# Optimization experiments

Measured on AMD Instinct MI355X. Metric: run time of the kernel, lower is better.

## Reference

```python
import jax, jax.numpy as jnp
import numpy as np

W_PRIOR_STD = 1.0          # w_prior_stddev
OBS_STD = 1.0              # observational_noise_stddev
EPS = 1e-7                 # keras backend.epsilon()
B, E, K, C = 64, 32, 128, 512


def setup_inputs() -> dict:
    key = jax.random.key(0)
    k1, k2, k3, k4 = jax.random.split(key, 4)
    x = jax.random.normal(k1, (B, E, C), jnp.float32)
    prior_memory_mean = jax.random.normal(k2, (K, C), jnp.float32)  # truncated_normal(0,1) init
    prior_log_variance_scale = jax.random.uniform(k3, (), jnp.float32)  # scalar weight (init zeros; nonzero for testing)
    log_w_stddev = jnp.float32(0.3)  # constant(initial_w_stddev) init
    z_noise = jax.random.normal(k4, (E, B, C), jnp.float32)  # reparam noise for z_distribution.sample()
    return {"x": x, "prior_memory_mean": prior_memory_mean,
            "prior_log_variance_scale": prior_log_variance_scale,
            "log_w_stddev": log_w_stddev, "z_noise": z_noise}


def _kl_w(w, sw, k):
    # KL( N(w, sw^2 I_k) || N(0, w_prior^2 I_k) ), w_prior = 1
    return 0.5 * (k * sw * sw + jnp.sum(w * w, axis=-1) - k - 2.0 * k * jnp.log(sw))


def reference(x, prior_memory_mean, prior_log_variance_scale, log_w_stddev, z_noise):
    b, e, c = x.shape
    k = prior_memory_mean.shape[0]
    dt = x.dtype
    sw = jnp.exp(log_w_stddev)                      # w_stddev
    lam = (OBS_STD ** 2) / (W_PRIOR_STD ** 2)       # l2 regularizer in w-solve
    I_k = jnp.eye(k, dtype=dt)

    # prior state (tiled over batch)
    M0 = jnp.broadcast_to(prior_memory_mean[None], (b, k, c)) + jnp.zeros((b, k, c), dt)
    var = prior_log_variance_scale + EPS
    U0 = jnp.broadcast_to(var * I_k, (b, k, k)) + jnp.zeros((b, k, k), dt)

    z = jnp.transpose(x, (1, 0, 2))  # [E,B,C]

    def solve_w(M, z_t):
        # least squares: w = (M M^T + lam I)^{-1} M z  -> [B,K]
        A = jnp.einsum('bkc,blc->bkl', M, M) + lam * I_k
        rhs = jnp.einsum('bkc,bc->bk', M, z_t)
        return jnp.linalg.solve(A, rhs[..., None])[..., 0]

    def step(carry, z_t):
        M, U = carry                                    # [B,K,C], [B,K,K]
        w = solve_w(M, z_t)                             # memory sample == mean; iteration_count == 1
        delta = z_t - jnp.einsum('bk,bkc->bc', w, M)    # prediction delta [B,C]
        wU = jnp.einsum('bk,bkl->bl', w, U)             # cross variance [B,K]
        sigma = jnp.sum(wU * w, axis=-1) + OBS_STD ** 2 # z episode covariance [B]
        gain = wU / sigma[:, None]                      # [B,K]
        M_new = M + gain[..., None] * delta[:, None, :] # rank-1 Kalman update
        U_new = U - jnp.einsum('bk,bl->bkl', gain, wU)
        return (M_new, U_new), _kl_w(w, sw, k)          # per-step w divergence [B]

    (M_post, U_post), kl_episode = jax.lax.scan(step, (M0, U0), z)  # kl_episode [E,B]

    # read memory: batched solve with shared Gram matrix over episode
    A = jnp.einsum('bkc,blc->bkl', M_post, M_post) + lam * I_k
    rhs = jnp.einsum('bkc,ebc->bke', M_post, z)
    w_read = jnp.transpose(jnp.linalg.solve(A, rhs), (2, 0, 1))     # [E,B,K]
    z_mean = jnp.einsum('ebk,bkc->ebc', w_read, M_post)
    kl_read = _kl_w(w_read, sw, k)                                  # [E,B]

    total_divergence = jnp.mean(kl_episode + kl_read)               # add_loss value
    z_sample = z_mean + OBS_STD * z_noise                           # reparameterized sample
    return jnp.transpose(z_sample, (1, 0, 2)), total_divergence
```

## Files before the change

kernel.cpp:

```cpp
#include <hip/hip_runtime.h>

#define BB 64
#define EE 32
#define KK 128
#define CC 512
#define V0EPS 1e-7f

#define LTR 132
#define PTS 132
#define LKM 36
#define L36 36
#define LWT 176
#define SEG(i) ((((i) >> 4) * 20) + ((i) & 15))

#define SC_S2  0
#define SC_SIG 1
#define SC_KL  2
#define SC_B1  3
#define SC_B2  4
#define SC_R11 5
#define SC_R12 6
#define SC_R22 7

__device__ __forceinline__ float wsum64(float v) {
#pragma unroll
  for (int m = 32; m >= 1; m >>= 1) v += __shfl_xor(v, m, 64);
  return v;
}

__device__ __forceinline__ float wsum32(float v) {
#pragma unroll
  for (int m = 16; m >= 1; m >>= 1) v += __shfl_xor(v, m, 64);
  return v;
// ... 203 lines not shown
          if (q == (j2 >> 4)) sFb[dn][i][r] = wv_;
          if (r == j2) {
#pragma unroll
            for (int c = 0; c < 16; c++) {
              sPv[dn][i][16 * q + c] = wreg[c];
              sPv[dn][i][128 + 16 * q + c] = vreg[c];
            }
          }
        }
      }
      __syncthreads();
    }
    {
      float dval = 0.0f;
#pragma unroll
      for (int c = 0; c < 16; c++) if (c == (r & 15)) dval = wreg[c];
      if (q == (r >> 4)) sFb[0][0][r] = dval;
    }
    __syncthreads();
    {
      const float sc = 1.0f / sFb[0][0][r];
      float4* o4 = (float4*)(Ainv0 + r * KK + 16 * q);
#pragma unroll
      for (int u = 0; u < 4; u++) {
        float4 o;
        o.x = vreg[4 * u] * sc; o.y = vreg[4 * u + 1] * sc;
        o.z = vreg[4 * u + 2] * sc; o.w = vreg[4 * u + 3] * sc;
        o4[u] = o;
      }
    }
  }
}

__global__ __launch_bounds__(512) void scan_kernel(
    const float* __restrict__ Pg, const float* __restrict__ Sg,
    const float* __restrict__ scaleP, const float* __restrict__ Ainv0,
    float* __restrict__ wsKL, float* __restrict__ wsKLr, float* __restrict__ wsWt) {
  __shared__ __align__(16) float sPT[EE * PTS];
  __shared__ __align__(16) float sGT[EE * LTR];
  __shared__ __align__(16) float sEggT[EE * LTR];
  __shared__ __align__(16) float uni2[EE * LTR];
  __shared__ __align__(16) float uni3[KK * LKM];
  __shared__ __align__(16) float uni1[KK * LKM];
  __shared__ __align__(16) float sEk[KK * LKM];
  __shared__ __align__(16) float sS[EE * L36];
  __shared__ __align__(16) float sD[EE * L36];
  __shared__ __align__(16) float sW[160];
  __shared__ __align__(16) float sWU[160];
  __shared__ __align__(16) float sPu[160];
  __shared__ __align__(16) float sPm[160];
  __shared__ __align__(16) float sQ[160];
  __shared__ __align__(16) float sDz[EE];
  __shared__ __align__(16) float sDgw[EE];
  __shared__ __align__(16) float sQt[EE];
  __shared__ __align__(16) float sScal[16];

  float* sYT = uni2;
  float* sGk = uni3;
  float* sYk = uni1;

  const int tid = threadIdx.x, wv = tid >> 6, ln = tid & 63;
  const int mr = tid >> 2, mq = tid & 3;
  const int b = blockIdx.x;

  float areg[32];
  {
    const float4* a4 = (const float4*)(Ainv0 + mr * KK + 32 * mq);
#pragma unroll
    for (int u = 0; u < 8; u++) {
      const float4 t4 = a4[u];
      areg[4 * u] = t4.x; areg[4 * u + 1] = t4.y; areg[4 * u + 2] = t4.z; areg[4 * u + 3] = t4.w;
    }
  }
  {
    const float* Pb = Pg + (size_t)b * KK * EE;
#pragma unroll
    for (int i = 0; i < 8; i++) {
      const int idx = tid + 512 * i;
      sPT[(idx & 31) * PTS + (idx >> 5)] = Pb[idx];
    }
    const float* Sb = Sg + (size_t)b * 4096;
#pragma unroll
    for (int i = 0; i < 2; i++) {
      const int idx = tid + 512 * i;
      sS[(idx >> 5) * L36 + (idx & 31)] =
          Sb[idx] + Sb[idx + 1024] + Sb[idx + 2048] + Sb[idx + 3072];
    }
  }
  if (tid < 16) sScal[tid] = 0.0f;
  const float v0 = scaleP[0] + V0EPS;
  __syncthreads();
  {
    const float* xb = sPT + 32 * mq;
    float s = 0;
#pragma unroll
    for (int c = 0; c < 32; c++) s += areg[c] * xb[c];
    s += __shfl_xor(s, 1, 64); s += __shfl_xor(s, 2, 64);
    if (mq == 0) sW[SEG(mr)] = s;
  }
  __syncthreads();

#pragma unroll 1
  for (int t = 0; t < EE; ++t) {
    const bool hn = (t + 1 < EE);
    {
      const float* xb = sW + 40 * mq;
      float s = 0;
#pragma unroll
      for (int c = 0; c < 16; c++) s += areg[c] * xb[c];
#pragma unroll
      for (int c = 0; c < 16; c++) s += areg[16 + c] * xb[20 + c];
      s += __shfl_xor(s, 1, 64); s += __shfl_xor(s, 2, 64);
      if (mq == 0) sPm[SEG(mr)] = s;
    }
    if (tid < 256) {
      const int s8 = tid >> 3, p3 = tid & 7;
      if (s8 < t) {
        const float* gr = sGT + s8 * LTR + 16 * p3;
        const float* wr_ = sW + 20 * p3;
        float s = 0;
#pragma unroll
        for (int kk = 0; kk < 16; kk++) s += gr[kk] * wr_[kk];
        s += __shfl_xor(s, 1, 64); s += __shfl_xor(s, 2, 64); s += __shfl_xor(s, 4, 64);
        if (p3 == 0) sDgw[s8] = s;
      } else if (s8 == 31) {
        const float* wp = sW + 20 * p3;
        float s = 0;
#pragma unroll
        for (int kk = 0; kk < 16; kk++) s += wp[kk] * wp[kk];
        s += __shfl_xor(s, 1, 64); s += __shfl_xor(s, 2, 64); s += __shfl_xor(s, 4, 64);
        if (p3 == 0) sScal[SC_S2] = s;
      }
    } else {
      const int j = (tid - 256) >> 3, p3 = tid & 7;
      if (j < t) {
        const float* yr = sYT + j * LTR + 16 * p3;
        const float* wr_ = sW + 20 * p3;
        float s = 0;
#pragma unroll
        for (int kk = 0; kk < 16; kk++) s += yr[kk] * wr_[kk];
        s += __shfl_xor(s, 1, 64); s += __shfl_xor(s, 2, 64); s += __shfl_xor(s, 4, 64);
        if (p3 == 0) sQt[j] = s;
      }
    }
    __syncthreads();
    if (tid < 256) {
      const int k = tid >> 1, h = tid & 1;
      const float* yk = sYk + k * LKM + 16 * h;
      const float* qb = sQt + 16 * h;
      float a = 0;
#pragma unroll
      for (int u = 0; u < 16; u++) {
        const int j = 16 * h + u;
        a += (j < t) ? yk[u] * qb[u] : 0.0f;
      }
      a += __shfl_xor(a, 1, 64);
      if (h == 0) sWU[SEG(k)] = v0 * sW[SEG(k)] - a;
    } else if (tid < 384) {
      const int k = tid - 256;
      float a = sW[SEG(k)];
      const float* ek = sEk + k * LKM;
      const int nc = (t + 3) >> 2;
#pragma unroll 1
      for (int c4 = 0; c4 < nc; ++c4) {
        const float4 ev = *(const float4*)(ek + 4 * c4);
        const float4 dv = *(const float4*)(sDgw + 4 * c4);
        const int u0 = 4 * c4;
        a -= ((u0 + 0 < t) ? ev.x * dv.x : 0.0f) + ((u0 + 1 < t) ? ev.y * dv.y : 0.0f) +
             ((u0 + 2 < t) ? ev.z * dv.z : 0.0f) + ((u0 + 3 < t) ? ev.w * dv.w : 0.0f);
      }
      sEk[k * LKM + t] = a;
      sEggT[t * LTR + k] = a;
    } else if (tid < 448) {
      if (ln < 32) {
        const int r2 = ln;
        float a = (r2 == t) ? 1.0f : 0.0f;
        for (int s2 = 0; s2 < t; ++s2) a -= sDgw[s2] * sD[s2 * L36 + r2];
        sD[t * L36 + r2] = a;
      } else {
        const int k0 = (ln - 32) * 4;
        const float4 wv4 = *(const float4*)(sW + SEG(k0));
        const float4 pm4 = *(const float4*)(sPm + SEG(k0));
        float a = dot4(wv4, pm4);
        a = wsum32(a);
        if (ln == 32) sScal[SC_R22] = a;
      }
    } else {
      const float s2v = sScal[SC_S2];
      float a = (ln < t) ? sQt[ln] * sQt[ln] : 0.0f;
      a = wsum64(a);
      if (ln == 0) {
        sScal[SC_SIG] = v0 * s2v - a + 1.0f;
        sScal[SC_KL] += s2v;
      }
    }
    __syncthreads();
    {
      const float* xb = sWU + 40 * mq;
      float s = 0;
#pragma unroll
      for (int c = 0; c < 16; c++) s += areg[c] * xb[c];
#pragma unroll
      for (int c = 0; c < 16; c++) s += areg[16 + c] * xb[20 + c];
      s += __shfl_xor(s, 1, 64); s += __shfl_xor(s, 2, 64);
      if (mq == 0) sPu[SEG(mr)] = s;
    }
    if (tid < 256) {
      const int s4 = tid >> 3, p3 = tid & 7;
      if (hn && s4 <= t) {
        const float* er = sEggT + s4 * LTR + 16 * p3;
        const float* pr = sPT + (t + 1) * PTS + 16 * p3;
        float a = 0;
#pragma unroll
        for (int kk = 0; kk < 16; kk++) a -= er[kk] * pr[kk];
        const float4 dv = *(const float4*)(sD + s4 * L36 + 4 * p3);
        const float4 sv = *(const float4*)(sS + (t + 1) * L36 + 4 * p3);
        a += dot4(dv, sv);
        a += __shfl_xor(a, 1, 64); a += __shfl_xor(a, 2, 64); a += __shfl_xor(a, 4, 64);
        if (p3 == 0) sDz[s4] = a;
      }
    } else if (tid < 320) {
      float a = sEggT[t * LTR + ln] * sPT[t * PTS + ln] +
                sEggT[t * LTR + ln + 64] * sPT[t * PTS + ln + 64];
      a = wsum64(a);
      if (ln == 0) sScal[SC_B2] = a;
    } else if (tid < 384) {
      if (ln < 32) {
        float a = sD[t * L36 + ln] * sS[t * L36 + ln];
        a = wsum32(a);
        if (ln == 0) sScal[SC_B1] = a;
      } else {
        const int k0 = (ln - 32) * 4;
        const float4 wu4 = *(const float4*)(sWU + SEG(k0));
        const float4 pm4 = *(const float4*)(sPm + SEG(k0));
        float a = dot4(wu4, pm4);
        a = wsum32(a);
        if (ln == 32) sScal[SC_R12] = a;
      }
    } else if (tid < 448) {
      const float sig = sScal[SC_SIG];
      const float rsq = rsqrtf(sig);
#pragma unroll
      for (int u = 0; u < 2; u++) {
        const int k = ln + 64 * u;
        const float wu = sWU[SEG(k)];
        const float gv = wu / sig;
        const float yv = wu * rsq;
        sGT[t * LTR + k] = gv;
        sGk[k * LKM + t] = gv;
        sYT[t * LTR + k] = yv;
        sYk[k * LKM + t] = yv;
      }
    }
    __syncthreads();
    if (hn) {
      const float* gk = sGk + mr * LKM + 8 * mq;
      const float* dzb = sDz + 8 * mq;
      float a = 0;
#pragma unroll
      for (int u = 0; u < 8; u++) {
        const int s2 = 8 * mq + u;
        a += (s2 < t) ? gk[u] * dzb[u] : 0.0f;
      }
      a += __shfl_xor(a, 1, 64); a += __shfl_xor(a, 2, 64);
      if (mq == 0)
        sQ[SEG(mr)] = sPT[(t + 1) * PTS + mr] + a + (sWU[SEG(mr)] / sScal[SC_SIG]) * sDz[t];
    }
    if (wv == 0) {
      float a = sWU[SEG(ln)] * sPu[SEG(ln)] + sWU[SEG(ln + 64)] * sPu[SEG(ln + 64)];
      a = wsum64(a);
      if (ln == 0) sScal[SC_R11] = a;
    }
    __syncthreads();
    {
      const float4 sc0 = *(const float4*)(sScal);
      const float4 sc1 = *(const float4*)(sScal + 4);
      const float rs = 1.0f / sc0.y;
      const float beta = sc0.w - sc1.x - sc0.x;
      const float e11 = sc1.y * rs * rs;
      const float e12 = sc1.z * rs + 1.0f;
      const float e22 = sc1.w - beta;
      const float rd = 1.0f / (e11 * e22 - e12 * e12);
      const float t11 = e22 * rd, t12 = -e12 * rd, t22 = e11 * rd;
      const float u1r = sPu[SEG(mr)] * rs, u2r = sPm[SEG(mr)];
      const float* pub = sPu + 40 * mq;
      const float* pmb = sPm + 40 * mq;
#pragma unroll
      for (int c = 0; c < 16; c++) {
        const float u1c = pub[c] * rs;
        const float u2c = pmb[c];
        areg[c] -= u1r * (t11 * u1c + t12 * u2c) + u2r * (t12 * u1c + t22 * u2c);
      }
#pragma unroll
      for (int c = 0; c < 16; c++) {
        const float u1c = pub[20 + c] * rs;
        const float u2c = pmb[20 + c];
        areg[16 + c] -= u1r * (t11 * u1c + t12 * u2c) + u2r * (t12 * u1c + t22 * u2c);
      }
    }
    if (hn) {
      const float* xb = sQ + 40 * mq;
      float s = 0;
#pragma unroll
      for (int c = 0; c < 16; c++) s += areg[c] * xb[c];
#pragma unroll
      for (int c = 0; c < 16; c++) s += areg[16 + c] * xb[20 + c];
      s += __shfl_xor(s, 1, 64); s += __shfl_xor(s, 2, 64);
      if (mq == 0) sW[SEG(mr)] = s;
    }
    __syncthreads();
  }

  float* sR1T  = uni2;
  float* sGamT = uni2 + 1152;
  float* sRhsT = uni1;
  float* sWrT  = uni3;
  if (tid == 0) wsKL[b] = sScal[SC_KL];

#pragma unroll
  for (int h = 0; h < 2; ++h) {
    const int lin = tid + 512 * h, s = lin >> 5, e = lin & 31;
    const float4* er = (const float4*)(sEggT + s * LTR);
    const float4* pr = (const float4*)(sPT + e * PTS);
    float a = 0;
#pragma unroll 8
    for (int u = 0; u < 32; ++u) a -= dot4(er[u], pr[u]);
    const float4* dr = (const float4*)(sD + s * L36);
    const float4* sr = (const float4*)(sS + e * L36);
#pragma unroll
    for (int u = 0; u < 8; ++u) a += dot4(dr[u], sr[u]);
    sR1T[e * 36 + s] = a;
  }
  __syncthreads();
  {
    const int k = tid & 127, e4 = tid >> 7;
    float4 g0, g1, g2, g3, g4, g5, g6, g7;
    {
      const float4* gk = (const float4*)(sGk + k * LKM);
      g0 = gk[0]; g1 = gk[1]; g2 = gk[2]; g3 = gk[3];
      g4 = gk[4]; g5 = gk[5]; g6 = gk[6]; g7 = gk[7];
    }
#pragma unroll
    for (int u = 0; u < 8; ++u) {
      const int e = e4 * 8 + u;
      const float4* r1 = (const float4*)(sR1T + e * 36);
      float a = sPT[e * PTS + k];
      a += dot4(g0, r1[0]) + dot4(g1, r1[1]) + dot4(g2, r1[2]) + dot4(g3, r1[3]);
      a += dot4(g4, r1[4]) + dot4(g5, r1[5]) + dot4(g6, r1[6]) + dot4(g7, r1[7]);
      sRhsT[e * PTS + k] = a;
    }
  }
  __syncthreads();
#pragma unroll 2
  for (int e = 0; e < EE; ++e) {
    const float* xb = sRhsT + e * PTS + 32 * mq;
    float s = 0;
#pragma unroll
    for (int c = 0; c < 32; c++) s += areg[c] * xb[c];
    s += __shfl_xor(s, 1, 64); s += __shfl_xor(s, 2, 64);
    if (mq == 0) sWrT[e * PTS + mr] = s;
  }
  __syncthreads();
#pragma unroll
  for (int h = 0; h < 2; ++h) {
    const int lin = tid + 512 * h, s = lin >> 5, e = lin & 31;
    const float4* gr = (const float4*)(sGT + s * LTR);
    const float4* wr = (const float4*)(sWrT + e * PTS);
    float a = 0;
#pragma unroll 8
    for (int u = 0; u < 32; ++u) a += dot4(gr[u], wr[u]);
    sGamT[e * 36 + s] = a;
  }
  __syncthreads();
  {
    const int k = tid & 127, e4 = tid >> 7;
    float4 E0, E1, E2, E3, E4, E5, E6, E7;
    {
      const float4* ek = (const float4*)(sEk + k * LKM);
      E0 = ek[0]; E1 = ek[1]; E2 = ek[2]; E3 = ek[3];
      E4 = ek[4]; E5 = ek[5]; E6 = ek[6]; E7 = ek[7];
    }
#pragma unroll
    for (int u = 0; u < 8; ++u) {
      const int e = e4 * 8 + u;
      const float4* gm = (const float4*)(sGamT + e * 36);
      float a = sWrT[e * PTS + k];
      a -= dot4(E0, gm[0]) + dot4(E1, gm[1]) + dot4(E2, gm[2]) + dot4(E3, gm[3]);
      a -= dot4(E4, gm[4]) + dot4(E5, gm[5]) + dot4(E6, gm[6]) + dot4(E7, gm[7]);
      wsWt[(size_t)b * 5120 + e * 160 + k] = a;
    }
  }
  {
    const int e = tid & 31, sp = tid >> 5;
    float4 gm[8];
    {
      const float4* g4 = (const float4*)(sGamT + e * 36);
#pragma unroll
      for (int u = 0; u < 8; ++u) gm[u] = g4[u];
    }
#pragma unroll
    for (int h = 0; h < 2; ++h) {
      const int sp2 = sp + 16 * h;
      float a = 0;
#pragma unroll
      for (int u = 0; u < 8; ++u) {
        const float4 g = gm[u];
        a += sD[(4 * u + 0) * L36 + sp2] * g.x + sD[(4 * u + 1) * L36 + sp2] * g.y +
             sD[(4 * u + 2) * L36 + sp2] * g.z + sD[(4 * u + 3) * L36 + sp2] * g.w;
      }
      wsWt[(size_t)b * 5120 + e * 160 + 128 + sp2] = a;
    }
  }
  {
    const int e = tid >> 4, p = tid & 15;
    const float4* wr = (const float4*)(sWrT + e * PTS + 8 * p);
    const float4 w0 = wr[0], w1 = wr[1];
    float a = dot4(w0, w0) + dot4(w1, w1);
    a += __shfl_xor(a, 1, 64); a += __shfl_xor(a, 2, 64);
    a += __shfl_xor(a, 4, 64); a += __shfl_xor(a, 8, 64);
    if (p == 0) wsKLr[b * EE + e] = a;
  }
}

__global__ __launch_bounds__(512) void postBF_kernel(
    const float* __restrict__ wsWt, const float* __restrict__ x,
    const float* __restrict__ M0, const float* __restrict__ znoise,
    const float* __restrict__ wsKL, const float* __restrict__ wsKLr,
    const float* __restrict__ lwsP, float* __restrict__ out) {
  __shared__ __align__(16) float sWtT[32 * LWT];
  __shared__ __align__(16) float Mch[2 * 16 * 132];
  const int tid = threadIdx.x;

  if (blockIdx.x == 256) {
    float* sPp = sWtT;
    float s = 0.0f;
    if (tid < 64) s += wsKL[tid];
    for (int i = tid; i < 2048; i += 512) s += wsKLr[i];
    sPp[tid] = s;
    __syncthreads();
    for (int off = 256; off > 0; off >>= 1) {
      if (tid < off) sPp[tid] += sPp[tid + off];
      __syncthreads();
    }
    if (tid == 0) {
      const float lws = lwsP[0];
      const float sw2 = expf(2.0f * lws);
      out[(size_t)BB * EE * CC] =
          0.5f * sPp[0] / (float)(EE * BB) + (float)KK * (sw2 - 1.0f - 2.0f * lws);
    }
    return;
  }

  const int b = blockIdx.x >> 2, cq = blockIdx.x & 3;
  {
    const int e = tid >> 4, j = tid & 15;
    const float* Wg = wsWt + (size_t)b * 5120 + e * 160;
#pragma unroll
    for (int u = 0; u < 10; ++u) sWtT[e * LWT + j + 16 * u] = Wg[j + 16 * u];
  }
  const int srow = tid >> 5, sc4 = tid & 31;
  const int e = tid & 31, cs = tid >> 5;
  const float* xb = x + (size_t)b * EE * CC;
  const int cbase = cq * 128;
  float4 st = *(const float4*)(M0 + srow * CC + cbase + 4 * sc4);
  float acc[8];
#pragma unroll
  for (int u = 0; u < 8; u++) acc[u] = 0.0f;
  int buf = 0;
#pragma unroll 1
  for (int ch2 = 0; ch2 < 10; ++ch2) {
    *(float4*)(Mch + buf * 2112 + srow * 132 + 4 * sc4) = st;
    __syncthreads();
    if (ch2 + 1 < 10) {
      const int row = (ch2 + 1) * 16 + srow;
      st = (row < 128) ? *(const float4*)(M0 + row * CC + cbase + 4 * sc4)
                       : *(const float4*)(xb + (row - 128) * CC + cbase + 4 * sc4);
    }
    const float4* wt4 = (const float4*)(sWtT + e * LWT + ch2 * 16);
    const float4 wa = wt4[0], wb = wt4[1], wc = wt4[2], wd = wt4[3];
    const float wv16[16] = {wa.x, wa.y, wa.z, wa.w, wb.x, wb.y, wb.z, wb.w,
                            wc.x, wc.y, wc.z, wc.w, wd.x, wd.y, wd.z, wd.w};
#pragma unroll
    for (int kk = 0; kk < 16; ++kk) {
      const float* mrp = Mch + buf * 2112 + kk * 132 + cs * 8;
      const float4 m0 = *(const float4*)(mrp);
      const float4 m1 = *(const float4*)(mrp + 4);
      const float wk = wv16[kk];
      acc[0] += wk * m0.x; acc[1] += wk * m0.y; acc[2] += wk * m0.z; acc[3] += wk * m0.w;
      acc[4] += wk * m1.x; acc[5] += wk * m1.y; acc[6] += wk * m1.z; acc[7] += wk * m1.w;
    }
    buf ^= 1;
  }
  {
    const size_t ob = ((size_t)b * EE + e) * CC + cbase + cs * 8;
    const size_t nb = ((size_t)e * BB + b) * CC + cbase + cs * 8;
#pragma unroll
    for (int u = 0; u < 2; u++) {
      const float4 nz = *(const float4*)(znoise + nb + 4 * u);
      float4 o;
      o.x = acc[4 * u] + nz.x;     o.y = acc[4 * u + 1] + nz.y;
      o.z = acc[4 * u + 2] + nz.z; o.w = acc[4 * u + 3] + nz.w;
      *(float4*)(out + ob + 4 * u) = o;
    }
  }
}

extern "C" void kernel_launch(void* const* d_in, const int* in_sizes, int n_in,
                              void* d_out, int out_size, void* d_ws, size_t ws_size,
                              hipStream_t stream) {
  (void)in_sizes; (void)n_in; (void)out_size; (void)ws_size;
  const float* x = (const float*)d_in[0];
  const float* M0 = (const float*)d_in[1];
  const float* scaleP = (const float*)d_in[2];
  const float* lwsP = (const float*)d_in[3];
  const float* znoise = (const float*)d_in[4];
  float* out = (float*)d_out;

  float* ws = (float*)d_ws;
  float* wsP = ws;
  float* wsSp = wsP + 262144;
  float* wsA0 = wsSp + 262144;
  float* wsAinv0 = wsA0 + 16384;
  float* wsKL = wsAinv0 + 16384;
  float* wsKLr = wsKL + 64;
  float* wsWt = wsKLr + 2048;

  a0_kernel<<<512, 256, 0, stream>>>(M0, wsA0);
  psinv_kernel<<<257, 1024, 0, stream>>>(x, M0, wsP, wsSp, wsA0, wsAinv0);
  scan_kernel<<<BB, 512, 0, stream>>>(wsP, wsSp, scaleP, wsAinv0,
                                      wsKL, wsKLr, wsWt);
  postBF_kernel<<<257, 512, 0, stream>>>(wsWt, x, M0, znoise, wsKL, wsKLr, lwsP, out);
}
```

Measured before the change: 261.6 us.

## Fuse scan and post kernels into one cooperative launch with grid sync

Merges the per-batch scan kernel and the post-processing read/output kernel into a single cooperative kernel of 256 blocks, with the first 64 blocks running the scan and all blocks doing the output GEMM after a grid-wide barrier. Shared memory is carved from a single unified array so both phases can reuse it. The aim is to remove one kernel launch and its inter-kernel gap. In exchange it adds grid-sync overhead and requires all 256 blocks to be co-resident, and the post blocks now carry the scan kernel's large shared memory footprint.

```diff
diff --git a/kernel.cpp b/kernel.cpp
--- a/kernel.cpp
+++ b/kernel.cpp
@@ -1,4 +1,7 @@
 #include <hip/hip_runtime.h>
+#include <hip/hip_cooperative_groups.h>
+
+namespace cg = cooperative_groups;
 
 #define BB 64
 #define EE 32
@@ -268,407 +271,465 @@
   }
 }
 
-__global__ __launch_bounds__(512) void scan_kernel(
+__global__ __launch_bounds__(512) void scanpost_kernel(
     const float* __restrict__ Pg, const float* __restrict__ Sg,
     const float* __restrict__ scaleP, const float* __restrict__ Ainv0,
-    float* __restrict__ wsKL, float* __restrict__ wsKLr, float* __restrict__ wsWt) {
-  __shared__ __align__(16) float sPT[EE * PTS];
-  __shared__ __align__(16) float sGT[EE * LTR];
-  __shared__ __align__(16) float sEggT[EE * LTR];
-  __shared__ __align__(16) float uni2[EE * LTR];
-  __shared__ __align__(16) float uni3[KK * LKM];
-  __shared__ __align__(16) float uni1[KK * LKM];
-  __shared__ __align__(16) float sEk[KK * LKM];
-  __shared__ __align__(16) float sS[EE * L36];
-  __shared__ __align__(16) float sD[EE * L36];
-  __shared__ __align__(16) float sW[160];
-  __shared__ __align__(16) float sWU[160];
-  __shared__ __align__(16) float sPu[160];
-  __shared__ __align__(16) float sPm[160];
-  __shared__ __align__(16) float sQ[160];
-  __shared__ __align__(16) float sDz[EE];
-  __shared__ __align__(16) float sDgw[EE];
-  __shared__ __align__(16) float sQt[EE];
-  __shared__ __align__(16) float sScal[16];
-
-  float* sYT = uni2;
-  float* sGk = uni3;
-  float* sYk = uni1;
-
-  const int tid = threadIdx.x, wv = tid >> 6, ln = tid & 63;
-  const int mr = tid >> 2, mq = tid & 3;
-  const int b = blockIdx.x;
-
-  float areg[32];
-  {
-    const float4* a4 = (const float4*)(Ainv0 + mr * KK + 32 * mq);
-#pragma unroll
-    for (int u = 0; u < 8; u++) {
-      const float4 t4 = a4[u];
-      areg[4 * u] = t4.x; areg[4 * u + 1] = t4.y; areg[4 * u + 2] = t4.z; areg[4 * u + 3] = t4.w;
-    }
-  }
-  {
-    const float* Pb = Pg + (size_t)b * KK * EE;
-#pragma unroll
-    for (int i = 0; i < 8; i++) {
-      const int idx = tid + 512 * i;
-      sPT[(idx & 31) * PTS + (idx >> 5)] = Pb[idx];
-    }
-    const float* Sb = Sg + (size_t)b * 4096;
-#pragma unroll
-    for (int i = 0; i < 2; i++) {
-      const int idx = tid + 512 * i;
-      sS[(idx >> 5) * L36 + (idx & 31)] =
-          Sb[idx] + Sb[idx + 1024] + Sb[idx + 2048] + Sb[idx + 3072];
-    }
-  }
-  if (tid < 16) sScal[tid] = 0.0f;
-  const float v0 = scaleP[0] + V0EPS;
-  __syncthreads();
-  {
-    const float* xb = sPT + 32 * mq;
-    float s = 0;
-#pragma unroll
-    for (int c = 0; c < 32; c++) s += areg[c] * xb[c];
-    s += __shfl_xor(s, 1, 64); s += __shfl_xor(s, 2, 64);
-    if (mq == 0) sW[SEG(mr)] = s;
-  }
-  __syncthreads();
-
-#pragma unroll 1
-  for (int t = 0; t < EE; ++t) {
-    const bool hn = (t + 1 < EE);
-    {
-      const float* xb = sW + 40 * mq;
+    float* __restrict__ wsKL, float* __restrict__ wsKLr, float* __restrict__ wsWt,
+    const float* __restrict__ x, const float* __restrict__ M0,
+    const float* __restrict__ znoise, const float* __restrict__ lwsP,
+    float* __restrict__ out) {
+  __shared__ __align__(16) float SM[33936];
+  const int tid = threadIdx.x;
+
+  if (blockIdx.x < 64) {
+    float* sPT   = SM;
+    float* sGT   = SM + 4224;
+    float* sEggT = SM + 8448;
+    float* uni2  = SM + 12672;
+    float* uni3  = SM + 16896;
+    float* uni1  = SM + 21504;
+    float* sEk   = SM + 26112;
+    float* sS    = SM + 30720;
+    float* sD    = SM + 31872;
+    float* sW    = SM + 33024;
+    float* sWU   = SM + 33184;
+    float* sPu   = SM + 33344;
+    float* sPm   = SM + 33504;
+    float* sQ    = SM + 33664;
+    float* sDz   = SM + 33824;
+    float* sDgw  = SM + 33856;
+    float* sQt   = SM + 33888;
+    float* sScal = SM + 33920;
+    float* sYT = uni2;
+    float* sGk = uni3;
+    float* sYk = uni1;
+
+    const int wv = tid >> 6, ln = tid & 63;
+    const int mr = tid >> 2, mq = tid & 3;
+    const int b = blockIdx.x;
+
+    float areg[32];
+    {
+      const float4* a4 = (const float4*)(Ainv0 + mr * KK + 32 * mq);
+#pragma unroll
+      for (int u = 0; u < 8; u++) {
+        const float4 t4 = a4[u];
+        areg[4 * u] = t4.x; areg[4 * u + 1] = t4.y; areg[4 * u + 2] = t4.z; areg[4 * u + 3] = t4.w;
+      }
+    }
+    {
+      const float* Pb = Pg + (size_t)b * KK * EE;
+#pragma unroll
+      for (int i = 0; i < 8; i++) {
+        const int idx = tid + 512 * i;
+        sPT[(idx & 31) * PTS + (idx >> 5)] = Pb[idx];
+      }
+      const float* Sb = Sg + (size_t)b * 4096;
+#pragma unroll
+      for (int i = 0; i < 2; i++) {
+        const int idx = tid + 512 * i;
+        sS[(idx >> 5) * L36 + (idx & 31)] =
+            Sb[idx] + Sb[idx + 1024] + Sb[idx + 2048] + Sb[idx + 3072];
+      }
+    }
+    if (tid < 16) sScal[tid] = 0.0f;
+    const float v0 = scaleP[0] + V0EPS;
+    __syncthreads();
+    {
+      const float* xb = sPT + 32 * mq;
       float s = 0;
 #pragma unroll
-      for (int c = 0; c < 16; c++) s += areg[c] * xb[c];
-#pragma unroll
-      for (int c = 0; c < 16; c++) s += areg[16 + c] * xb[20 + c];
-      s += __shfl_xor(s, 1, 64); s += __shfl_xor(s, 2, 64);
-      if (mq == 0) sPm[SEG(mr)] = s;
-    }
-    if (tid < 256) {
-      const int s8 = tid >> 3, p3 = tid & 7;
-      if (s8 < t) {
-        const float* gr = sGT + s8 * LTR + 16 * p3;
-        const float* wr_ = sW + 20 * p3;
-        float s = 0;
-#pragma unroll
-        for (int kk = 0; kk < 16; kk++) s += gr[kk] * wr_[kk];
-        s += __shfl_xor(s, 1, 64); s += __shfl_xor(s, 2, 64); s += __shfl_xor(s, 4, 64);
-        if (p3 == 0) sDgw[s8] = s;
-      } else if (s8 == 31) {
-        const float* wp = sW + 20 * p3;
-        float s = 0;
-#pragma unroll
-        for (int kk = 0; kk < 16; kk++) s += wp[kk] * wp[kk];
-        s += __shfl_xor(s, 1, 64); s += __shfl_xor(s, 2, 64); s += __shfl_xor(s, 4, 64);
-        if (p3 == 0) sScal[SC_S2] = s;
-      }
-    } else {
-      const int j = (tid - 256) >> 3, p3 = tid & 7;
-      if (j < t) {
-        const float* yr = sYT + j * LTR + 16 * p3;
-        const float* wr_ = sW + 20 * p3;
-        float s = 0;
-#pragma unroll
-        for (int kk = 0; kk < 16; kk++) s += yr[kk] * wr_[kk];
-        s += __shfl_xor(s, 1, 64); s += __shfl_xor(s, 2, 64); s += __shfl_xor(s, 4, 64);
-        if (p3 == 0) sQt[j] = s;
-      }
-    }
-    __syncthreads();
-    if (tid < 256) {
-      const int k = tid >> 1, h = tid & 1;
-      const float* yk = sYk + k * LKM + 16 * h;
-      const float* qb = sQt + 16 * h;
-      float a = 0;
-#pragma unroll
-      for (int u = 0; u < 16; u++) {
-        const int j = 16 * h + u;
-        a += (j < t) ? yk[u] * qb[u] : 0.0f;
-      }
-      a += __shfl_xor(a, 1, 64);
-      if (h == 0) sWU[SEG(k)] = v0 * sW[SEG(k)] - a;
-    } else if (tid < 384) {
-      const int k = tid - 256;
-      float a = sW[SEG(k)];
-      const float* ek = sEk + k * LKM;
-      const int nc = (t + 3) >> 2;
-#pragma unroll 1
-      for (int c4 = 0; c4 < nc; ++c4) {
-        const float4 ev = *(const float4*)(ek + 4 * c4);
-        const float4 dv = *(const float4*)(sDgw + 4 * c4);
-        const int u0 = 4 * c4;
-        a -= ((u0 + 0 < t) ? ev.x * dv.x : 0.0f) + ((u0 + 1 < t) ? ev.y * dv.y : 0.0f) +
-             ((u0 + 2 < t) ? ev.z * dv.z : 0.0f) + ((u0 + 3 < t) ? ev.w * dv.w : 0.0f);
-      }
-      sEk[k * LKM + t] = a;
-      sEggT[t * LTR + k] = a;
-    } else if (tid < 448) {
-      if (ln < 32) {
-        const int r2 = ln;
-        float a = (r2 == t) ? 1.0f : 0.0f;
-        for (int s2 = 0; s2 < t; ++s2) a -= sDgw[s2] * sD[s2 * L36 + r2];
-        sD[t * L36 + r2] = a;
-      } else {
-        const int k0 = (ln - 32) * 4;
-        const float4 wv4 = *(const float4*)(sW + SEG(k0));
-        const float4 pm4 = *(const float4*)(sPm + SEG(k0));
-        float a = dot4(wv4, pm4);
-        a = wsum32(a);
-        if (ln == 32) sScal[SC_R22] = a;
-      }
-    } else {
-      const float s2v = sScal[SC_S2];
-      float a = (ln < t) ? sQt[ln] * sQt[ln] : 0.0f;
-      a = wsum64(a);
-      if (ln == 0) {
-        sScal[SC_SIG] = v0 * s2v - a + 1.0f;
-        sScal[SC_KL] += s2v;
-      }
-    }
-    __syncthreads();
-    {
-      const float* xb = sWU + 40 * mq;
-      float s = 0;
-#pragma unroll
-      for (int c = 0; c < 16; c++) s += areg[c] * xb[c];
-#pragma unroll
-      for (int c = 0; c < 16; c++) s += areg[16 + c] * xb[20 + c];
-      s += __shfl_xor(s, 1, 64); s += __shfl_xor(s, 2, 64);
-      if (mq == 0) sPu[SEG(mr)] = s;
-    }
-    if (tid < 256) {
-      const int s4 = tid >> 3, p3 = tid & 7;
-      if (hn && s4 <= t) {
-        const float* er = sEggT + s4 * LTR + 16 * p3;
-        const float* pr = sPT + (t + 1) * PTS + 16 * p3;
-        float a = 0;
-#pragma unroll
-        for (int kk = 0; kk < 16; kk++) a -= er[kk] * pr[kk];
-        const float4 dv = *(const float4*)(sD + s4 * L36 + 4 * p3);
-        const float4 sv = *(const float4*)(sS + (t + 1) * L36 + 4 * p3);
-        a += dot4(dv, sv);
-        a += __shfl_xor(a, 1, 64); a += __shfl_xor(a, 2, 64); a += __shfl_xor(a, 4, 64);
-        if (p3 == 0) sDz[s4] = a;
-      }
-    } else if (tid < 320) {
-      float a = sEggT[t * LTR + ln] * sPT[t * PTS + ln] +
-                sEggT[t * LTR + ln + 64] * sPT[t * PTS + ln + 64];
-      a = wsum64(a);
-      if (ln == 0) sScal[SC_B2] = a;
-    } else if (tid < 384) {
-      if (ln < 32) {
-        float a = sD[t * L36 + ln] * sS[t * L36 + ln];
-        a = wsum32(a);
-        if (ln == 0) sScal[SC_B1] = a;
-      } else {
-        const int k0 = (ln - 32) * 4;
-        const float4 wu4 = *(const float4*)(sWU + SEG(k0));
-        const float4 pm4 = *(const float4*)(sPm + SEG(k0));
-        float a = dot4(wu4, pm4);
-        a = wsum32(a);
-        if (ln == 32) sScal[SC_R12] = a;
-      }
-    } else if (tid < 448) {
-      const float sig = sScal[SC_SIG];
-      const float rsq = rsqrtf(sig);
-#pragma unroll
-      for (int u = 0; u < 2; u++) {
-        const int k = ln + 64 * u;
-        const float wu = sWU[SEG(k)];
-        const float gv = wu / sig;
-        const float yv = wu * rsq;
-        sGT[t * LTR + k] = gv;
-        sGk[k * LKM + t] = gv;
-        sYT[t * LTR + k] = yv;
-        sYk[k * LKM + t] = yv;
-      }
-    }
-    __syncthreads();
-    if (hn) {
-      const float* gk = sGk + mr * LKM + 8 * mq;
-      const float* dzb = sDz + 8 * mq;
-      float a = 0;
-#pragma unroll
-      for (int u = 0; u < 8; u++) {
-        const int s2 = 8 * mq + u;
-        a += (s2 < t) ? gk[u] * dzb[u] : 0.0f;
-      }
-      a += __shfl_xor(a, 1, 64); a += __shfl_xor(a, 2, 64);
-      if (mq == 0)
-        sQ[SEG(mr)] = sPT[(t + 1) * PTS + mr] + a + (sWU[SEG(mr)] / sScal[SC_SIG]) * sDz[t];
-    }
-    if (wv == 0) {
-      float a = sWU[SEG(ln)] * sPu[SEG(ln)] + sWU[SEG(ln + 64)] * sPu[SEG(ln + 64)];
-      a = wsum64(a);
-      if (ln == 0) sScal[SC_R11] = a;
-    }
-    __syncthreads();
-    {
-      const float4 sc0 = *(const float4*)(sScal);
-      const float4 sc1 = *(const float4*)(sScal + 4);
-      const float rs = 1.0f / sc0.y;
-      const float beta = sc0.w - sc1.x - sc0.x;
-      const float e11 = sc1.y * rs * rs;
-      const float e12 = sc1.z * rs + 1.0f;
-      const float e22 = sc1.w - beta;
-      const float rd = 1.0f / (e11 * e22 - e12 * e12);
-      const float t11 = e22 * rd, t12 = -e12 * rd, t22 = e11 * rd;
-      const float u1r = sPu[SEG(mr)] * rs, u2r = sPm[SEG(mr)];
-      const float* pub = sPu + 40 * mq;
-      const float* pmb = sPm + 40 * mq;
-#pragma unroll
-      for (int c = 0; c < 16; c++) {
-        const float u1c = pub[c] * rs;
-        const float u2c = pmb[c];
-        areg[c] -= u1r * (t11 * u1c + t12 * u2c) + u2r * (t12 * u1c + t22 * u2c);
-      }
-#pragma unroll
-      for (int c = 0; c < 16; c++) {
-        const float u1c = pub[20 + c] * rs;
-        const float u2c = pmb[20 + c];
-        areg[16 + c] -= u1r * (t11 * u1c + t12 * u2c) + u2r * (t12 * u1c + t22 * u2c);
-      }
-    }
-    if (hn) {
-      const float* xb = sQ + 40 * mq;
-      float s = 0;
-#pragma unroll
-      for (int c = 0; c < 16; c++) s += areg[c] * xb[c];
-#pragma unroll
-      for (int c = 0; c < 16; c++) s += areg[16 + c] * xb[20 + c];
+      for (int c = 0; c < 32; c++) s += areg[c] * xb[c];
       s += __shfl_xor(s, 1, 64); s += __shfl_xor(s, 2, 64);
       if (mq == 0) sW[SEG(mr)] = s;
     }
     __syncthreads();
+
+#pragma unroll 1
+    for (int t = 0; t < EE; ++t) {
+      const bool hn = (t + 1 < EE);
+      {
+        const float* xb = sW + 40 * mq;
+        float s = 0;
+#pragma unroll
+        for (int c = 0; c < 16; c++) s += areg[c] * xb[c];
+#pragma unroll
+        for (int c = 0; c < 16; c++) s += areg[16 + c] * xb[20 + c];
+        s += __shfl_xor(s, 1, 64); s += __shfl_xor(s, 2, 64);
+        if (mq == 0) sPm[SEG(mr)] = s;
+      }
+      if (tid < 256) {
+        const int s8 = tid >> 3, p3 = tid & 7;
+        if (s8 < t) {
+          const float* gr = sGT + s8 * LTR + 16 * p3;
+          const float* wr_ = sW + 20 * p3;
+          float s = 0;
+#pragma unroll
+          for (int kk = 0; kk < 16; kk++) s += gr[kk] * wr_[kk];
+          s += __shfl_xor(s, 1, 64); s += __shfl_xor(s, 2, 64); s += __shfl_xor(s, 4, 64);
+          if (p3 == 0) sDgw[s8] = s;
+        } else if (s8 == 31) {
+          const float* wp = sW + 20 * p3;
+          float s = 0;
+#pragma unroll
+          for (int kk = 0; kk < 16; kk++) s += wp[kk] * wp[kk];
+          s += __shfl_xor(s, 1, 64); s += __shfl_xor(s, 2, 64); s += __shfl_xor(s, 4, 64);
+          if (p3 == 0) sScal[SC_S2] = s;
+        }
+      } else {
+        const int j = (tid - 256) >> 3, p3 = tid & 7;
+        if (j < t) {
+          const float* yr = sYT + j * LTR + 16 * p3;
+          const float* wr_ = sW + 20 * p3;
+          float s = 0;
+#pragma unroll
+          for (int kk = 0; kk < 16; kk++) s += yr[kk] * wr_[kk];
+          s += __shfl_xor(s, 1, 64); s += __shfl_xor(s, 2, 64); s += __shfl_xor(s, 4, 64);
+          if (p3 == 0) sQt[j] = s;
+        }
+      }
+      __syncthreads();
+      if (tid < 256) {
+        const int k = tid >> 1, h = tid & 1;
+        const float* yk = sYk + k * LKM + 16 * h;
+        const float* qb = sQt + 16 * h;
+        float a = 0;
+#pragma unroll
+        for (int u = 0; u < 16; u++) {
+          const int j = 16 * h + u;
+          a += (j < t) ? yk[u] * qb[u] : 0.0f;
+        }
+        a += __shfl_xor(a, 1, 64);
+        if (h == 0) sWU[SEG(k)] = v0 * sW[SEG(k)] - a;
+      } else if (tid < 384) {
+        const int k = tid - 256;
+        float a = sW[SEG(k)];
+        const float* ek = sEk + k * LKM;
+        const int nc = (t + 3) >> 2;
+#pragma unroll 1
+        for (int c4 = 0; c4 < nc; ++c4) {
+          const float4 ev = *(const float4*)(ek + 4 * c4);
+          const float4 dv = *(const float4*)(sDgw + 4 * c4);
+          const int u0 = 4 * c4;
+          a -= ((u0 + 0 < t) ? ev.x * dv.x : 0.0f) + ((u0 + 1 < t) ? ev.y * dv.y : 0.0f) +
+               ((u0 + 2 < t) ? ev.z * dv.z : 0.0f) + ((u0 + 3 < t) ? ev.w * dv.w : 0.0f);
+        }
+        sEk[k * LKM + t] = a;
+        sEggT[t * LTR + k] = a;
+      } else if (tid < 448) {
+        if (ln < 32) {
+          const int r2 = ln;
+          float a = (r2 == t) ? 1.0f : 0.0f;
+          for (int s2 = 0; s2 < t; ++s2) a -= sDgw[s2] * sD[s2 * L36 + r2];
+          sD[t * L36 + r2] = a;
+        } else {
+          const int k0 = (ln - 32) * 4;
+          const float4 wv4 = *(const float4*)(sW + SEG(k0));
+          const float4 pm4 = *(const float4*)(sPm + SEG(k0));
+          float a = dot4(wv4, pm4);
+          a = wsum32(a);
+          if (ln == 32) sScal[SC_R22] = a;
+        }
+      } else {
+        const float s2v = sScal[SC_S2];
+        float a = (ln < t) ? sQt[ln] * sQt[ln] : 0.0f;
+        a = wsum64(a);
+        if (ln == 0) {
+          sScal[SC_SIG] = v0 * s2v - a + 1.0f;
+          sScal[SC_KL] += s2v;
+        }
+      }
+      __syncthreads();
+      {
+        const float* xb = sWU + 40 * mq;
+        float s = 0;
+#pragma unroll
+        for (int c = 0; c < 16; c++) s += areg[c] * xb[c];
+#pragma unroll
+        for (int c = 0; c < 16; c++) s += areg[16 + c] * xb[20 + c];
+        s += __shfl_xor(s, 1, 64); s += __shfl_xor(s, 2, 64);
+        if (mq == 0) sPu[SEG(mr)] = s;
+      }
+      if (tid < 256) {
+        const int s4 = tid >> 3, p3 = tid & 7;
+        if (hn && s4 <= t) {
+          const float* er = sEggT + s4 * LTR + 16 * p3;
+          const float* pr = sPT + (t + 1) * PTS + 16 * p3;
+          float a = 0;
+#pragma unroll
+          for (int kk = 0; kk < 16; kk++) a -= er[kk] * pr[kk];
+          const float4 dv = *(const float4*)(sD + s4 * L36 + 4 * p3);
+          const float4 sv = *(const float4*)(sS + (t + 1) * L36 + 4 * p3);
+          a += dot4(dv, sv);
+          a += __shfl_xor(a, 1, 64); a += __shfl_xor(a, 2, 64); a += __shfl_xor(a, 4, 64);
+          if (p3 == 0) sDz[s4] = a;
+        }
+      } else if (tid < 320) {
+        float a = sEggT[t * LTR + ln] * sPT[t * PTS + ln] +
+                  sEggT[t * LTR + ln + 64] * sPT[t * PTS + ln + 64];
+        a = wsum64(a);
+        if (ln == 0) sScal[SC_B2] = a;
+      } else if (tid < 384) {
+        if (ln < 32) {
+          float a = sD[t * L36 + ln] * sS[t * L36 + ln];
+          a = wsum32(a);
+          if (ln == 0) sScal[SC_B1] = a;
+        } else {
+          const int k0 = (ln - 32) * 4;
+          const float4 wu4 = *(const float4*)(sWU + SEG(k0));
+          const float4 pm4 = *(const float4*)(sPm + SEG(k0));
+          float a = dot4(wu4, pm4);
+          a = wsum32(a);
+          if (ln == 32) sScal[SC_R12] = a;
+        }
+      } else if (tid < 448) {
+        const float sig = sScal[SC_SIG];
+        const float rsq = rsqrtf(sig);
+#pragma unroll
+        for (int u = 0; u < 2; u++) {
+          const int k = ln + 64 * u;
+          const float wu = sWU[SEG(k)];
+          const float gv = wu / sig;
+          const float yv = wu * rsq;
+          sGT[t * LTR + k] = gv;
+          sGk[k * LKM + t] = gv;
+          sYT[t * LTR + k] = yv;
+          sYk[k * LKM + t] = yv;
+        }
+      }
+      __syncthreads();
+      if (hn) {
+        const float* gk = sGk + mr * LKM + 8 * mq;
+        const float* dzb = sDz + 8 * mq;
+        float a = 0;
+#pragma unroll
+        for (int u = 0; u < 8; u++) {
+          const int s2 = 8 * mq + u;
+          a += (s2 < t) ? gk[u] * dzb[u] : 0.0f;
+        }
+        a += __shfl_xor(a, 1, 64); a += __shfl_xor(a, 2, 64);
+        if (mq == 0)
+          sQ[SEG(mr)] = sPT[(t + 1) * PTS + mr] + a + (sWU[SEG(mr)] / sScal[SC_SIG]) * sDz[t];
+      }
+      if (wv == 0) {
+        float a = sWU[SEG(ln)] * sPu[SEG(ln)] + sWU[SEG(ln + 64)] * sPu[SEG(ln + 64)];
+        a = wsum64(a);
+        if (ln == 0) sScal[SC_R11] = a;
+      }
+      __syncthreads();
+      {
+        const float4 sc0 = *(const float4*)(sScal);
+        const float4 sc1 = *(const float4*)(sScal + 4);
+        const float rs = 1.0f / sc0.y;
+        const float beta = sc0.w - sc1.x - sc0.x;
+        const float e11 = sc1.y * rs * rs;
+        const float e12 = sc1.z * rs + 1.0f;
+        const float e22 = sc1.w - beta;
+        const float rd = 1.0f / (e11 * e22 - e12 * e12);
+        const float t11 = e22 * rd, t12 = -e12 * rd, t22 = e11 * rd;
+        const float u1r = sPu[SEG(mr)] * rs, u2r = sPm[SEG(mr)];
+        const float* pub = sPu + 40 * mq;
+        const float* pmb = sPm + 40 * mq;
+#pragma unroll
+        for (int c = 0; c < 16; c++) {
+          const float u1c = pub[c] * rs;
+          const float u2c = pmb[c];
+          areg[c] -= u1r * (t11 * u1c + t12 * u2c) + u2r * (t12 * u1c + t22 * u2c);
+        }
+#pragma unroll
+        for (int c = 0; c < 16; c++) {
+          const float u1c = pub[20 + c] * rs;
+          const float u2c = pmb[20 + c];
+          areg[16 + c] -= u1r * (t11 * u1c + t12 * u2c) + u2r * (t12 * u1c + t22 * u2c);
+        }
+      }
+      if (hn) {
+        const float* xb = sQ + 40 * mq;
+        float s = 0;
+#pragma unroll
+        for (int c = 0; c < 16; c++) s += areg[c] * xb[c];
+#pragma unroll
+        for (int c = 0; c < 16; c++) s += areg[16 + c] * xb[20 + c];
+        s += __shfl_xor(s, 1, 64); s += __shfl_xor(s, 2, 64);
+        if (mq == 0) sW[SEG(mr)] = s;
+      }
+      __syncthreads();
+    }
+
+    float* sR1T  = uni2;
+    float* sGamT = uni2 + 1152;
+    float* sRhsT = uni1;
+    float* sWrT  = uni3;
+    if (tid == 0) wsKL[b] = sScal[SC_KL];
+
+#pragma unroll
+    for (int h = 0; h < 2; ++h) {
+      const int lin = tid + 512 * h, s = lin >> 5, e = lin & 31;
+      const float4* er = (const float4*)(sEggT + s * LTR);
+      const float4* pr = (const float4*)(sPT + e * PTS);
+      float a = 0;
+#pragma unroll 8
+      for (int u = 0; u < 32; ++u) a -= dot4(er[u], pr[u]);
+      const float4* dr = (const float4*)(sD + s * L36);
+      const float4* sr = (const float4*)(sS + e * L36);
+#pragma unroll
+      for (int u = 0; u < 8; ++u) a += dot4(dr[u], sr[u]);
+      sR1T[e * 36 + s] = a;
+    }
+    __syncthreads();
+    {
+      const int k = tid & 127, e4 = tid >> 7;
+      float4 g0, g1, g2, g3, g4, g5, g6, g7;
+      {
+        const float4* gk = (const float4*)(sGk + k * LKM);
+        g0 = gk[0]; g1 = gk[1]; g2 = gk[2]; g3 = gk[3];
+        g4 = gk[4]; g5 = gk[5]; g6 = gk[6]; g7 = gk[7];
+      }
+#pragma unroll
+      for (int u = 0; u < 8; ++u) {
+        const int e = e4 * 8 + u;
+        const float4* r1 = (const float4*)(sR1T + e * 36);
+        float a = sPT[e * PTS + k];
+        a += dot4(g0, r1[0]) + dot4(g1, r1[1]) + dot4(g2, r1[2]) + dot4(g3, r1[3]);
+        a += dot4(g4, r1[4]) + dot4(g5, r1[5]) + dot4(g6, r1[6]) + dot4(g7, r1[7]);
+        sRhsT[e * PTS + k] = a;
+      }
+    }
+    __syncthreads();
+#pragma unroll 2
+    for (int e = 0; e < EE; ++e) {
+      const float* xb = sRhsT + e * PTS + 32 * mq;
+      float s = 0;
+#pragma unroll
+      for (int c = 0; c < 32; c++) s += areg[c] * xb[c];
+      s += __shfl_xor(s, 1, 64); s += __shfl_xor(s, 2, 64);
+      if (mq == 0) sWrT[e * PTS + mr] = s;
+    }
+    __syncthreads();
+#pragma unroll
+    for (int h = 0; h < 2; ++h) {
+      const int lin = tid + 512 * h, s = lin >> 5, e = lin & 31;
+      const float4* gr = (const float4*)(sGT + s * LTR);
+      const float4* wr = (const float4*)(sWrT + e * PTS);
+      float a = 0;
+#pragma unroll 8
+      for (int u = 0; u < 32; ++u) a += dot4(gr[u], wr[u]);
+      sGamT[e * 36 + s] = a;
+    }
+    __syncthreads();
+    {
+      const int k = tid & 127, e4 = tid >> 7;
+      float4 E0, E1, E2, E3, E4, E5, E6, E7;
+      {
+        const float4* ek = (const float4*)(sEk + k * LKM);
+        E0 = ek[0]; E1 = ek[1]; E2 = ek[2]; E3 = ek[3];
+        E4 = ek[4]; E5 = ek[5]; E6 = ek[6]; E7 = ek[7];
+      }
+#pragma unroll
+      for (int u = 0; u < 8; ++u) {
+        const int e = e4 * 8 + u;
+        const float4* gm = (const float4*)(sGamT + e * 36);
+        float a = sWrT[e * PTS + k];
+        a -= dot4(E0, gm[0]) + dot4(E1, gm[1]) + dot4(E2, gm[2]) + dot4(E3, gm[3]);
+        a -= dot4(E4, gm[4]) + dot4(E5, gm[5]) + dot4(E6, gm[6]) + dot4(E7, gm[7]);
+        wsWt[(size_t)b * 5120 + e * 160 + k] = a;
+      }
+    }
+    {
+      const int e = tid & 31, sp = tid >> 5;
+      float4 gm[8];
+      {
+        const float4* g4 = (const float4*)(sGamT + e * 36);
+#pragma unroll
+        for (int u = 0; u < 8; ++u) gm[u] = g4[u];
+      }
+#pragma unroll
+      for (int h = 0; h < 2; ++h) {
+        const int sp2 = sp + 16 * h;
+        float a = 0;
+#pragma unroll
+        for (int u = 0; u < 8; ++u) {
+          const float4 g = gm[u];
+          a += sD[(4 * u + 0) * L36 + sp2] * g.x + sD[(4 * u + 1) * L36 + sp2] * g.y +
+               sD[(4 * u + 2) * L36 + sp2] * g.z + sD[(4 * u + 3) * L36 + sp2] * g.w;
+        }
+        wsWt[(size_t)b * 5120 + e * 160 + 128 + sp2] = a;
+      }
+    }
+    {
+      const int e = tid >> 4, p = tid & 15;
+      const float4* wr = (const float4*)(sWrT + e * PTS + 8 * p);
+      const float4 w0 = wr[0], w1 = wr[1];
+      float a = dot4(w0, w0) + dot4(w1, w1);
+      a += __shfl_xor(a, 1, 64); a += __shfl_xor(a, 2, 64);
+      a += __shfl_xor(a, 4, 64); a += __shfl_xor(a, 8, 64);
+      if (p == 0) wsKLr[b * EE + e] = a;
+    }
+    __threadfence();
   }
 
-  float* sR1T  = uni2;
-  float* sGamT = uni2 + 1152;
-  float* sRhsT = uni1;
-  float* sWrT  = uni3;
-  if (tid == 0) wsKL[b] = sScal[SC_KL];
-
-#pragma unroll
-  for (int h = 0; h < 2; ++h) {
-    const int lin = tid + 512 * h, s = lin >> 5, e = lin & 31;
-    const float4* er = (const float4*)(sEggT + s * LTR);
-    const float4* pr = (const float4*)(sPT + e * PTS);
-    float a = 0;
-#pragma unroll 8
-    for (int u = 0; u < 32; ++u) a -= dot4(er[u], pr[u]);
-    const float4* dr = (const float4*)(sD + s * L36);
-    const float4* sr = (const float4*)(sS + e * L36);
-#pragma unroll
-    for (int u = 0; u < 8; ++u) a += dot4(dr[u], sr[u]);
-    sR1T[e * 36 + s] = a;
+  cg::this_grid().sync();
+
+  {
+    float* sWtT = SM;
+    float* Mch  = SM + 5632;
+    const int b = blockIdx.x >> 2, cq = blockIdx.x & 3;
+    {
+      const int e = tid >> 4, j = tid & 15;
+      const float* Wg = wsWt + (size_t)b * 5120 + e * 160;
+#pragma unroll
+      for (int u = 0; u < 10; ++u) sWtT[e * LWT + j + 16 * u] = Wg[j + 16 * u];
+    }
+    const int srow = tid >> 5, sc4 = tid & 31;
+    const int e = tid & 31, cs = tid >> 5;
+    const float* xb = x + (size_t)b * EE * CC;
+    const int cbase = cq * 128;
+    float4 st = *(const float4*)(M0 + srow * CC + cbase + 4 * sc4);
+    float acc[8];
+#pragma unroll
+    for (int u = 0; u < 8; u++) acc[u] = 0.0f;
+    int buf = 0;
+#pragma unroll 1
+    for (int ch2 = 0; ch2 < 10; ++ch2) {
+      *(float4*)(Mch + buf * 2112 + srow * 132 + 4 * sc4) = st;
+      __syncthreads();
+      if (ch2 + 1 < 10) {
+        const int row = (ch2 + 1) * 16 + srow;
+        st = (row < 128) ? *(const float4*)(M0 + row * CC + cbase + 4 * sc4)
+                         : *(const float4*)(xb + (row - 128) * CC + cbase + 4 * sc4);
+      }
+      const float4* wt4 = (const float4*)(sWtT + e * LWT + ch2 * 16);
+      const float4 wa = wt4[0], wb = wt4[1], wc = wt4[2], wd = wt4[3];
+      const float wv16[16] = {wa.x, wa.y, wa.z, wa.w, wb.x, wb.y, wb.z, wb.w,
+                              wc.x, wc.y, wc.z, wc.w, wd.x, wd.y, wd.z, wd.w};
+#pragma unroll
+      for (int kk = 0; kk < 16; ++kk) {
+        const float* mrp = Mch + buf * 2112 + kk * 132 + cs * 8;
+        const float4 m0 = *(const float4*)(mrp);
+        const float4 m1 = *(const float4*)(mrp + 4);
+        const float wk = wv16[kk];
+        acc[0] += wk * m0.x; acc[1] += wk * m0.y; acc[2] += wk * m0.z; acc[3] += wk * m0.w;
+        acc[4] += wk * m1.x; acc[5] += wk * m1.y; acc[6] += wk * m1.z; acc[7] += wk * m1.w;
+      }
+      buf ^= 1;
+    }
+    {
+      const size_t ob = ((size_t)b * EE + e) * CC + cbase + cs * 8;
+      const size_t nb = ((size_t)e * BB + b) * CC + cbase + cs * 8;
+#pragma unroll
+      for (int u = 0; u < 2; u++) {
+        const float4 nz = *(const float4*)(znoise + nb + 4 * u);
+        float4 o;
+        o.x = acc[4 * u] + nz.x;     o.y = acc[4 * u + 1] + nz.y;
+        o.z = acc[4 * u + 2] + nz.z; o.w = acc[4 * u + 3] + nz.w;
+        *(float4*)(out + ob + 4 * u) = o;
+      }
+    }
   }
-  __syncthreads();
-  {
-    const int k = tid & 127, e4 = tid >> 7;
-    float4 g0, g1, g2, g3, g4, g5, g6, g7;
-    {
-      const float4* gk = (const float4*)(sGk + k * LKM);
-      g0 = gk[0]; g1 = gk[1]; g2 = gk[2]; g3 = gk[3];
-      g4 = gk[4]; g5 = gk[5]; g6 = gk[6]; g7 = gk[7];
-    }
-#pragma unroll
-    for (int u = 0; u < 8; ++u) {
-      const int e = e4 * 8 + u;
-      const float4* r1 = (const float4*)(sR1T + e * 36);
-      float a = sPT[e * PTS + k];
-      a += dot4(g0, r1[0]) + dot4(g1, r1[1]) + dot4(g2, r1[2]) + dot4(g3, r1[3]);
-      a += dot4(g4, r1[4]) + dot4(g5, r1[5]) + dot4(g6, r1[6]) + dot4(g7, r1[7]);
-      sRhsT[e * PTS + k] = a;
-    }
-  }
-  __syncthreads();
-#pragma unroll 2
-  for (int e = 0; e < EE; ++e) {
-    const float* xb = sRhsT + e * PTS + 32 * mq;
-    float s = 0;
-#pragma unroll
-    for (int c = 0; c < 32; c++) s += areg[c] * xb[c];
-    s += __shfl_xor(s, 1, 64); s += __shfl_xor(s, 2, 64);
-    if (mq == 0) sWrT[e * PTS + mr] = s;
-  }
-  __syncthreads();
-#pragma unroll
-  for (int h = 0; h < 2; ++h) {
-    const int lin = tid + 512 * h, s = lin >> 5, e = lin & 31;
-    const float4* gr = (const float4*)(sGT + s * LTR);
-    const float4* wr = (const float4*)(sWrT + e * PTS);
-    float a = 0;
-#pragma unroll 8
-    for (int u = 0; u < 32; ++u) a += dot4(gr[u], wr[u]);
-    sGamT[e * 36 + s] = a;
-  }
-  __syncthreads();
-  {
-    const int k = tid & 127, e4 = tid >> 7;
-    float4 E0, E1, E2, E3, E4, E5, E6, E7;
-    {
-      const float4* ek = (const float4*)(sEk + k * LKM);
-      E0 = ek[0]; E1 = ek[1]; E2 = ek[2]; E3 = ek[3];
-      E4 = ek[4]; E5 = ek[5]; E6 = ek[6]; E7 = ek[7];
-    }
-#pragma unroll
-    for (int u = 0; u < 8; ++u) {
-      const int e = e4 * 8 + u;
-      const float4* gm = (const float4*)(sGamT + e * 36);
-      float a = sWrT[e * PTS + k];
-      a -= dot4(E0, gm[0]) + dot4(E1, gm[1]) + dot4(E2, gm[2]) + dot4(E3, gm[3]);
-      a -= dot4(E4, gm[4]) + dot4(E5, gm[5]) + dot4(E6, gm[6]) + dot4(E7, gm[7]);
-      wsWt[(size_t)b * 5120 + e * 160 + k] = a;
-    }
-  }
-  {
-    const int e = tid & 31, sp = tid >> 5;
-    float4 gm[8];
-    {
-      const float4* g4 = (const float4*)(sGamT + e * 36);
-#pragma unroll
-      for (int u = 0; u < 8; ++u) gm[u] = g4[u];
-    }
-#pragma unroll
-    for (int h = 0; h < 2; ++h) {
-      const int sp2 = sp + 16 * h;
-      float a = 0;
-#pragma unroll
-      for (int u = 0; u < 8; ++u) {
-        const float4 g = gm[u];
-        a += sD[(4 * u + 0) * L36 + sp2] * g.x + sD[(4 * u + 1) * L36 + sp2] * g.y +
-             sD[(4 * u + 2) * L36 + sp2] * g.z + sD[(4 * u + 3) * L36 + sp2] * g.w;
-      }
-      wsWt[(size_t)b * 5120 + e * 160 + 128 + sp2] = a;
-    }
-  }
-  {
-    const int e = tid >> 4, p = tid & 15;
-    const float4* wr = (const float4*)(sWrT + e * PTS + 8 * p);
-    const float4 w0 = wr[0], w1 = wr[1];
-    float a = dot4(w0, w0) + dot4(w1, w1);
-    a += __shfl_xor(a, 1, 64); a += __shfl_xor(a, 2, 64);
-    a += __shfl_xor(a, 4, 64); a += __shfl_xor(a, 8, 64);
-    if (p == 0) wsKLr[b * EE + e] = a;
-  }
-}
-
-__global__ __launch_bounds__(512) void postBF_kernel(
-    const float* __restrict__ wsWt, const float* __restrict__ x,
-    const float* __restrict__ M0, const float* __restrict__ znoise,
-    const float* __restrict__ wsKL, const float* __restrict__ wsKLr,
-    const float* __restrict__ lwsP, float* __restrict__ out) {
-  __shared__ __align__(16) float sWtT[32 * LWT];
-  __shared__ __align__(16) float Mch[2 * 16 * 132];
-  const int tid = threadIdx.x;
-
-  if (blockIdx.x == 256) {
-    float* sPp = sWtT;
+
+  if (blockIdx.x == 0) {
+    float* sPp = SM + 9856;
+    __syncthreads();
     float s = 0.0f;
     if (tid < 64) s += wsKL[tid];
     for (int i = tid; i < 2048; i += 512) s += wsKLr[i];
@@ -683,60 +744,6 @@
       const float sw2 = expf(2.0f * lws);
       out[(size_t)BB * EE * CC] =
           0.5f * sPp[0] / (float)(EE * BB) + (float)KK * (sw2 - 1.0f - 2.0f * lws);
-    }
-    return;
-  }
-
-  const int b = blockIdx.x >> 2, cq = blockIdx.x & 3;
-  {
-    const int e = tid >> 4, j = tid & 15;
-    const float* Wg = wsWt + (size_t)b * 5120 + e * 160;
-#pragma unroll
-    for (int u = 0; u < 10; ++u) sWtT[e * LWT + j + 16 * u] = Wg[j + 16 * u];
-  }
-  const int srow = tid >> 5, sc4 = tid & 31;
-  const int e = tid & 31, cs = tid >> 5;
-  const float* xb = x + (size_t)b * EE * CC;
-  const int cbase = cq * 128;
-  float4 st = *(const float4*)(M0 + srow * CC + cbase + 4 * sc4);
-  float acc[8];
-#pragma unroll
-  for (int u = 0; u < 8; u++) acc[u] = 0.0f;
-  int buf = 0;
-#pragma unroll 1
-  for (int ch2 = 0; ch2 < 10; ++ch2) {
-    *(float4*)(Mch + buf * 2112 + srow * 132 + 4 * sc4) = st;
-    __syncthreads();
-    if (ch2 + 1 < 10) {
-      const int row = (ch2 + 1) * 16 + srow;
-      st = (row < 128) ? *(const float4*)(M0 + row * CC + cbase + 4 * sc4)
-                       : *(const float4*)(xb + (row - 128) * CC + cbase + 4 * sc4);
-    }
-    const float4* wt4 = (const float4*)(sWtT + e * LWT + ch2 * 16);
-    const float4 wa = wt4[0], wb = wt4[1], wc = wt4[2], wd = wt4[3];
-    const float wv16[16] = {wa.x, wa.y, wa.z, wa.w, wb.x, wb.y, wb.z, wb.w,
-                            wc.x, wc.y, wc.z, wc.w, wd.x, wd.y, wd.z, wd.w};
-#pragma unroll
-    for (int kk = 0; kk < 16; ++kk) {
-      const float* mrp = Mch + buf * 2112 + kk * 132 + cs * 8;
-      const float4 m0 = *(const float4*)(mrp);
-      const float4 m1 = *(const float4*)(mrp + 4);
-      const float wk = wv16[kk];
-      acc[0] += wk * m0.x; acc[1] += wk * m0.y; acc[2] += wk * m0.z; acc[3] += wk * m0.w;
-      acc[4] += wk * m1.x; acc[5] += wk * m1.y; acc[6] += wk * m1.z; acc[7] += wk * m1.w;
-    }
-    buf ^= 1;
-  }
-  {
-    const size_t ob = ((size_t)b * EE + e) * CC + cbase + cs * 8;
-    const size_t nb = ((size_t)e * BB + b) * CC + cbase + cs * 8;
-#pragma unroll
-    for (int u = 0; u < 2; u++) {
-      const float4 nz = *(const float4*)(znoise + nb + 4 * u);
-      float4 o;
-      o.x = acc[4 * u] + nz.x;     o.y = acc[4 * u + 1] + nz.y;
-      o.z = acc[4 * u + 2] + nz.z; o.w = acc[4 * u + 3] + nz.w;
-      *(float4*)(out + ob + 4 * u) = o;
     }
   }
 }
@@ -763,7 +770,14 @@
 
   a0_kernel<<<512, 256, 0, stream>>>(M0, wsA0);
   psinv_kernel<<<257, 1024, 0, stream>>>(x, M0, wsP, wsSp, wsA0, wsAinv0);
-  scan_kernel<<<BB, 512, 0, stream>>>(wsP, wsSp, scaleP, wsAinv0,
-                                      wsKL, wsKLr, wsWt);
-  postBF_kernel<<<257, 512, 0, stream>>>(wsWt, x, M0, znoise, wsKL, wsKLr, lwsP, out);
+
+  const float* Pg = wsP;
+  const float* Sg = wsSp;
+  const float* Ainv0c = wsAinv0;
+  void* kargs[12] = {
+      (void*)&Pg, (void*)&Sg, (void*)&scaleP, (void*)&Ainv0c,
+      (void*)&wsKL, (void*)&wsKLr, (void*)&wsWt,
+      (void*)&x, (void*)&M0, (void*)&znoise, (void*)&lwsP, (void*)&out};
+  hipLaunchCooperativeKernel((void*)scanpost_kernel, dim3(256), dim3(512),
+                             kargs, 0, stream);
 }
```

Result: slower. 308.4 us (+17.9%).
